# Kernel tuning notes

Measured on AMD Instinct MI355X. Metric: run time of the kernel, lower is better.

The kernel has to match this reference:

```python
import jax, jax.numpy as jnp
import numpy as np
from jax import lax

B, CIN, COUT, K, SDIM = 4, 64, 128, 3, 512
D = H = W = 48


def setup_inputs() -> dict:
    key = jax.random.key(0)
    ks = jax.random.split(key, 8)
    inv = lambda n: 1.0 / np.sqrt(n)
    return {
        "x": jax.random.normal(ks[0], (B, CIN, D, H, W), jnp.float32),
        "style": jax.random.normal(ks[1], (B, SDIM), jnp.float32),
        "weight": jax.random.normal(ks[2], (COUT, CIN, K, K, K), jnp.float32),
        "bias": jnp.zeros((COUT,), jnp.float32),
        "w_scale": jax.random.uniform(ks[3], (CIN, SDIM), jnp.float32, -inv(SDIM), inv(SDIM)),
        "b_scale": jnp.zeros((CIN,), jnp.float32),
        "w_shift": jax.random.uniform(ks[4], (CIN, SDIM), jnp.float32, -inv(SDIM), inv(SDIM)),
        "b_shift": jnp.zeros((CIN,), jnp.float32),
        "w_kmod": jax.random.uniform(ks[5], (CIN * K ** 3, SDIM), jnp.float32, -inv(SDIM), inv(SDIM)),
        "b_kmod": jnp.zeros((CIN * K ** 3,), jnp.float32),
    }


def reference(x, style, weight, bias, w_scale, b_scale, w_shift, b_shift, w_kmod, b_kmod):
    # style-based per-channel input modulation: x * (1+scale) + shift
    scale = style @ w_scale.T + b_scale          # [B, CIN]
    shift = style @ w_shift.T + b_shift          # [B, CIN]
    xm = x * (1.0 + scale)[:, :, None, None, None] + shift[:, :, None, None, None]
    # per-sample kernel modulation: weight * (1 + kmod)
    kmod = (style @ w_kmod.T + b_kmod).reshape(B, CIN, K, K, K)
    w = weight[None] * (1.0 + kmod[:, None])     # [B, COUT, CIN, K, K, K]

    def conv_one(xi, wi):
        # xi: [CIN, D, H, W], wi: [COUT, CIN, K, K, K]
        return lax.conv_general_dilated(
            xi[None], wi, window_strides=(1, 1, 1), padding="SAME",
            dimension_numbers=("NCDHW", "OIDHW", "NCDHW"))[0]

    out = jax.vmap(conv_one)(xm, w)              # [B, COUT, D, H, W]
    return out + bias[None, :, None, None, None]
```

## Files before the change

kernel.cpp:

```cpp
#include <hip/hip_runtime.h>
#include <hip/hip_bf16.h>

#define NB   4
#define CIN  64
#define COUT 128
#define SDIM 512
#define DIM  48
#define SP   (DIM*DIM*DIM)
#define TAPS 27
#define KTOT (CIN*TAPS)

#define WS_S1P 0
#define WS_SH  (WS_S1P + NB*CIN)
#define WS_KM  (WS_SH + NB*CIN)
#define XPB_OFF   32768ull
#define XPB_BYTES (4ull*125000ull*64ull*2ull)
#define WSBF_OFF  (XPB_OFF + XPB_BYTES)
#define WSBF_BYTES ((size_t)NB*27*8*128*8*2)

typedef __attribute__((ext_vector_type(4))) float  f32x4;
typedef __attribute__((ext_vector_type(8))) short  short8;
typedef __attribute__((ext_vector_type(8))) unsigned short u16x8;

__device__ __forceinline__ void gld16(const void* g, void* l) {
    __builtin_amdgcn_global_load_lds(
        (const __attribute__((address_space(1))) void*)g,
        (__attribute__((address_space(3))) void*)l, 16, 0, 0);
}

__global__ void modparams_kernel(const float* __restrict__ style,
                                 const float* __restrict__ w_scale, const float* __restrict__ b_scale,
                                 const float* __restrict__ w_shift, const float* __restrict__ b_shift,
                                 const float* __restrict__ w_kmod,  const float* __restrict__ b_kmod,
                                 float* __restrict__ ws) {
    const int ROWS = 2 * CIN + CIN * TAPS;
    int gwave = (blockIdx.x * blockDim.x + threadIdx.x) >> 6;
    int lane  = threadIdx.x & 63;
    if (gwave >= NB * ROWS) return;
    int b = gwave / ROWS;
    int r = gwave % ROWS;

    const float* srow = style + b * SDIM;
    const float* mrow;
    float bias, add = 0.f;
    float* dst;
    if (r < CIN) {
        mrow = w_scale + r * SDIM; bias = b_scale[r];
        dst = ws + WS_S1P + b * CIN + r; add = 1.f;
    } else if (r < 2 * CIN) {
        int c = r - CIN;
        mrow = w_shift + c * SDIM; bias = b_shift[c];
        dst = ws + WS_SH + b * CIN + c;
    } else {
        int t = r - 2 * CIN;
        mrow = w_kmod + t * SDIM; bias = b_kmod[t];
        dst = ws + WS_KM + b * (CIN * TAPS) + t;
    }

    const float4* s4 = (const float4*)srow;
    const float4* m4 = (const float4*)mrow;
    float acc = 0.f;
    #pragma unroll
    for (int k4 = 0; k4 < 2; ++k4) {
        float4 sv = s4[lane + k4 * 64];
        float4 mv = m4[lane + k4 * 64];
        acc += sv.x * mv.x + sv.y * mv.y + sv.z * mv.z + sv.w * mv.w;
    }
    #pragma unroll
    for (int off = 32; off; off >>= 1) acc += __shfl_down(acc, off);
    if (lane == 0) *dst = acc + bias + add;
}

__global__ void build_wsbf2_kernel(const float* __restrict__ weight, const float* __restrict__ ws,
                                   unsigned short* __restrict__ wsbf) {
    int d = blockIdx.x * blockDim.x + threadIdx.x;
    if (d >= NB * 27 * 8 * 128 * 8) return;
    int j   = d & 7;
    int o   = (d >> 3) & 127;
    int s   = (d >> 10) & 7;
    int rem = d >> 13;
    int tau = rem % 27;
    int b   = rem / 27;
    int c   = s * 8 + j;
    float wm = weight[(o * CIN + c) * TAPS + tau] * (1.f + ws[WS_KM + b * KTOT + c * TAPS + tau]);
    __hip_bfloat16 h = __float2bfloat16(wm);
    wsbf[d] = *(unsigned short*)&h;
}

__global__ __launch_bounds__(256) void pad_kernel(const float* __restrict__ x,
                                                  const float* __restrict__ ws,
                                                  unsigned short* __restrict__ xpb) {
    __shared__ unsigned short lxm[48 * 72];
    int bid = blockIdx.x;
    int py = bid % 50;
    int pz = (bid / 50) % 50;
    int b  = bid / 2500;
    int t = threadIdx.x;
    bool interior = (pz >= 1 && pz <= 48 && py >= 1 && py <= 48);
    if (interior) {
        int z = pz - 1, y = py - 1;
        const float* xr = x + (size_t)b * CIN * SP + (size_t)z * (DIM*DIM) + y * DIM;
        #pragma unroll
        for (int it = 0; it < 3; ++it) {
            int u = it * 256 + t;
            int c  = u / 12;
            int w4 = (u - c * 12) * 4;
            float4 v = *(const float4*)(xr + (size_t)c * SP + w4);
            float s1 = ws[WS_S1P + b * CIN + c];
            float sh = ws[WS_SH  + b * CIN + c];
            float m0 = v.x * s1 + sh, m1 = v.y * s1 + sh;
            float m2 = v.z * s1 + sh, m3 = v.w * s1 + sh;
            __hip_bfloat16 h0 = __float2bfloat16(m0);
            __hip_bfloat16 h1 = __float2bfloat16(m1);
            __hip_bfloat16 h2 = __float2bfloat16(m2);
            __hip_bfloat16 h3 = __float2bfloat16(m3);
            lxm[(w4 + 0) * 72 + c] = *(unsigned short*)&h0;
            lxm[(w4 + 1) * 72 + c] = *(unsigned short*)&h1;
            lxm[(w4 + 2) * 72 + c] = *(unsigned short*)&h2;
            lxm[(w4 + 3) * 72 + c] = *(unsigned short*)&h3;
        }
    }
    __syncthreads();
    unsigned short* dst = xpb + (size_t)b * 8000000ull + ((size_t)pz * 2500 + py * 50) * 64;
    #pragma unroll
    for (int it = 0; it < 2; ++it) {
        int i8 = it * 256 + t;
        if (i8 < 400) {
            int w  = i8 >> 3;
            int c8 = (i8 & 7) * 8;
            u16x8 v = {};
            if (interior && w >= 1 && w <= 48)
                v = *(const u16x8*)&lxm[(w - 1) * 72 + c8];
            *(u16x8*)(dst + i8 * 8) = v;
        }
    }
}

#define HALOPOS 600
#define BH_CHUNKS (HALOPOS*8)

#define GLD16R(dst, p, OFF)                                                    \
    asm volatile("global_load_dwordx4 %0, %1, off offset:" #OFF                \
                 : "=v"(dst) : "v"(p) : "memory")

#define ISSUEA(buf, tap_) do {                                                 \
    const unsigned short* _p0 = wA + (size_t)(tap_) * 8192;                    \
    const unsigned short* _p1 = _p0 + 4096;                                    \
    GLD16R(buf[0], _p0, 0);   GLD16R(buf[1], _p0, 256);                        \
    GLD16R(buf[2], _p0, 512); GLD16R(buf[3], _p0, 768);                        \
    GLD16R(buf[4], _p1, 0);   GLD16R(buf[5], _p1, 256);                        \
    GLD16R(buf[6], _p1, 512); GLD16R(buf[7], _p1, 768);                        \
} while (0)

#define DLT(t_) (((t_) / 9) * 100 + (((t_) / 3) % 3) * 10 + ((t_) % 3))

#define BREADX(dst, bb, t_) do {                                               \
    _Pragma("unroll")                                                          \
    for (int nf = 0; nf < 4; ++nf) {                                           \
        const int D = DLT(t_) + nf * 20;                                       \
        dst[nf] = *(const short8*)((const char*)Bh + bb[D & 7] + D * 128);     \
    }                                                                          \
} while (0)

#define TAPP(cur, nxt, bcur, bnxt, t_) do {                                    \
    if ((t_) < 26) {                                                           \
        ISSUEA(nxt, (t_) + 1);                                                 \
        asm volatile("s_waitcnt vmcnt(8)" ::: "memory");                       \
    } else {                                                                   \
        asm volatile("s_waitcnt vmcnt(0)" ::: "memory");                       \
    }                                                                          \
    __builtin_amdgcn_sched_barrier(0);                                         \
    BREADX(bC1, bb1, t_);                       \
    _Pragma("unroll")                                                          \
    for (int mf = 0; mf < 4; ++mf)                                             \
        _Pragma("unroll")                                                      \
        for (int nf = 0; nf < 4; ++nf)                                         \
            acc[mf][nf] = __builtin_amdgcn_mfma_f32_16x16x32_bf16(             \
                cur[mf], bcur[nf], acc[mf][nf], 0, 0, 0);                      \
    if ((t_) < 26) BREADX(bnxt, bb0, (t_) + 1);       \
    _Pragma("unroll")                                                          \
    for (int mf = 0; mf < 4; ++mf)                                             \
        _Pragma("unroll")                                                      \
        for (int nf = 0; nf < 4; ++nf)                                         \
            acc[mf][nf] = __builtin_amdgcn_mfma_f32_16x16x32_bf16(             \
                cur[4 + mf], bC1[nf], acc[mf][nf], 0, 0, 0);                   \
} while (0)

__global__ __launch_bounds__(512, 2) void conv_fast15_kernel(
    const unsigned short* __restrict__ xpb,
    const unsigned short* __restrict__ wsbf,
    const float* __restrict__ bias,
    float* __restrict__ out)
{
    __shared__ unsigned short Bh[HALOPOS * 64];

    const int t    = threadIdx.x;
    const int lane = t & 63;
    const int wid  = t >> 6;
    const int wz   = wid & 3;
    const int mh   = wid >> 2;

    int bid0 = blockIdx.x;
    int bid  = (bid0 & 7) * 216 + (bid0 >> 3);
    int tile = bid % 432;
    int b    = bid / 432;
    int tx = tile % 6;
    int ty = (tile / 6) % 6;
    int tz = tile / 36;
    int x0 = tx * 8, y0 = ty * 8, z0 = tz * 4;

    const unsigned short* xb = xpb + (size_t)b * 8000000ull;
    const unsigned short* wb = wsbf + (size_t)b * (27 * 8 * 128 * 8);

    const int col  = lane & 15;
    const int krow = lane >> 4;
    const int cy   = col >> 3;
    const int cx   = col & 7;
    const int pbase = wz * 100 + cy * 10 + cx;

    const unsigned short* wA = wb + (size_t)(krow * 128 + mh * 64 + col) * 8;

    unsigned bb0[8], bb1[8];
    #pragma unroll
    for (int j = 0; j < 8; ++j) {
        int pj = (pbase + j) & 7;
        bb0[j] = (unsigned)(pbase * 128 + ((krow ^ pj) << 4));
        bb1[j] = (unsigned)(pbase * 128 + (((4 + krow) ^ pj) << 4));
    }

    f32x4 acc[4][4] = {};
    short8 a0[8], a1[8];
    short8 bX[4], bY[4], bC1[4];

    ISSUEA(a0, 0);

    #pragma unroll
    for (int it = 0; it < 10; ++it) {
        int i = it * 512 + t;
        if (i < BH_CHUNKS) {
            int pidx = i >> 3;
            int slot = i & 7;
            int hx = pidx % 10;
            int hy = (pidx / 10) % 10;
            int hz = pidx / 100;
            int srcslot = slot ^ (pidx & 7);
            const unsigned short* g = xb
                + ((size_t)((z0 + hz) * 2500 + (y0 + hy) * 50 + (x0 + hx))) * 64
                + srcslot * 8;
            gld16(g, &Bh[i * 8]);
        }
    }
    __syncthreads();

    BREADX(bX, bb0, 0);

    #pragma unroll
    for (int tp = 0; tp < 26; tp += 2) {
        TAPP(a0, a1, bX, bY, tp);
        TAPP(a1, a0, bY, bX, tp + 1);
    }
    TAPP(a0, a1, bX, bY, 26);

    int z  = z0 + wz;
    int xx = x0 + cx;
    #pragma unroll
    for (int mf = 0; mf < 4; ++mf) {
        f32x4 bv = *(const f32x4*)&bias[mh * 64 + mf * 16 + krow * 4];
        #pragma unroll
        for (int nf = 0; nf < 4; ++nf) {
            int y = y0 + nf * 2 + cy;
            size_t p = (size_t)z * (DIM * DIM) + (size_t)y * DIM + xx;
            f32x4 a = acc[mf][nf];
            #pragma unroll
            for (int r = 0; r < 4; ++r) {
                int o = mh * 64 + mf * 16 + krow * 4 + r;
                out[(size_t)(b * COUT + o) * SP + p] = a[r] + bv[r];
            }
        }
    }
}

extern "C" void kernel_launch(void* const* d_in, const int* in_sizes, int n_in,
                              void* d_out, int out_size, void* d_ws, size_t ws_size,
                              hipStream_t stream) {
    const float* x       = (const float*)d_in[0];
    const float* style   = (const float*)d_in[1];
    const float* weight  = (const float*)d_in[2];
    const float* bias    = (const float*)d_in[3];
    const float* w_scale = (const float*)d_in[4];
    const float* b_scale = (const float*)d_in[5];
    const float* w_shift = (const float*)d_in[6];
    const float* b_shift = (const float*)d_in[7];
    const float* w_kmod  = (const float*)d_in[8];
    const float* b_kmod  = (const float*)d_in[9];
    float* out = (float*)d_out;
    float* ws  = (float*)d_ws;

    unsigned short* xpb  = (unsigned short*)((char*)d_ws + XPB_OFF);
    unsigned short* wsbf = (unsigned short*)((char*)d_ws + WSBF_OFF);

    {
        int waves = NB * (2 * CIN + CIN * TAPS);
        int blocks = (waves + 3) / 4;
        modparams_kernel<<<blocks, 256, 0, stream>>>(style, w_scale, b_scale,
                                                     w_shift, b_shift, w_kmod, b_kmod, ws);
    }
    {
        int n = NB * 27 * 8 * 128 * 8;
        build_wsbf2_kernel<<<(n + 255) / 256, 256, 0, stream>>>(weight, ws, wsbf);
    }
    {
        int blocks = NB * 50 * 50;
        pad_kernel<<<blocks, 256, 0, stream>>>(x, ws, xpb);
    }
    {
        int blocks = NB * 432;
        conv_fast15_kernel<<<blocks, 512, 0, stream>>>(xpb, wsbf, bias, out);
    }
}
```

Measured before the change: 217.6 us.

## Stage only half the input channels in LDS, load the rest from global

The conv kernel now stages only the first 32 input channels of the halo tile in shared memory. The second half of the B operand is fetched straight from global memory per tap and software-pipelined alongside the weight loads. This halves LDS footprint and staging traffic, which may allow more blocks per CU and a shorter prologue. The cost is extra global/L2 traffic and more outstanding vector memory ops and registers per tap.

New measurement: 348.6 us. 60.2% more time.

```diff
diff --git a/kernel.cpp b/kernel.cpp
--- a/kernel.cpp
+++ b/kernel.cpp
@@ -137,7 +137,7 @@
 }
 
 #define HALOPOS 600
-#define BH_CHUNKS (HALOPOS*8)
+#define BH_CHUNKS (HALOPOS*4)
 
 #define GLD16R(dst, p, OFF)                                                    \
     asm volatile("global_load_dwordx4 %0, %1, off offset:" #OFF                \
@@ -153,46 +153,55 @@
 } while (0)
 
 #define DLT(t_) (((t_) / 9) * 100 + (((t_) / 3) % 3) * 10 + ((t_) % 3))
-
-#define BREADX(dst, bb, t_) do {                                               \
+#define DLTGB(t_) ((((t_) / 9) * 2500 + (((t_) / 3) % 3) * 50 + ((t_) % 3)) * 128)
+
+#define ISSUEB1G(buf, tap_) do {                                               \
+    _Pragma("unroll")                                                          \
+    for (int nf = 0; nf < 4; ++nf) {                                           \
+        const char* _pg = (const char*)xw1p[nf] + DLTGB(tap_);                 \
+        GLD16R(buf[nf], _pg, 0);                                               \
+    }                                                                          \
+} while (0)
+
+#define BREADX(dst, t_) do {                                                   \
     _Pragma("unroll")                                                          \
     for (int nf = 0; nf < 4; ++nf) {                                           \
         const int D = DLT(t_) + nf * 20;                                       \
-        dst[nf] = *(const short8*)((const char*)Bh + bb[D & 7] + D * 128);     \
+        dst[nf] = *(const short8*)((const char*)Bh + bb0[D & 3] + D * 64);     \
     }                                                                          \
 } while (0)
 
-#define TAPP(cur, nxt, bcur, bnxt, t_) do {                                    \
+#define TAPP(curA, nxtA, bcur, bnxt, bGc, bGn, t_) do {                        \
     if ((t_) < 26) {                                                           \
-        ISSUEA(nxt, (t_) + 1);                                                 \
-        asm volatile("s_waitcnt vmcnt(8)" ::: "memory");                       \
+        ISSUEA(nxtA, (t_) + 1);                                                \
+        ISSUEB1G(bGn, (t_) + 1);                                               \
+        asm volatile("s_waitcnt vmcnt(12)" ::: "memory");                      \
     } else {                                                                   \
         asm volatile("s_waitcnt vmcnt(0)" ::: "memory");                       \
     }                                                                          \
     __builtin_amdgcn_sched_barrier(0);                                         \
-    BREADX(bC1, bb1, t_);                       \
     _Pragma("unroll")                                                          \
     for (int mf = 0; mf < 4; ++mf)                                             \
         _Pragma("unroll")                                                      \
         for (int nf = 0; nf < 4; ++nf)                                         \
             acc[mf][nf] = __builtin_amdgcn_mfma_f32_16x16x32_bf16(             \
-                cur[mf], bcur[nf], acc[mf][nf], 0, 0, 0);                      \
-    if ((t_) < 26) BREADX(bnxt, bb0, (t_) + 1);       \
+                curA[mf], bcur[nf], acc[mf][nf], 0, 0, 0);                     \
+    if ((t_) < 26) BREADX(bnxt, (t_) + 1);            \
     _Pragma("unroll")                                                          \
     for (int mf = 0; mf < 4; ++mf)                                             \
         _Pragma("unroll")                                                      \
         for (int nf = 0; nf < 4; ++nf)                                         \
             acc[mf][nf] = __builtin_amdgcn_mfma_f32_16x16x32_bf16(             \
-                cur[4 + mf], bC1[nf], acc[mf][nf], 0, 0, 0);                   \
+                curA[4 + mf], bGc[nf], acc[mf][nf], 0, 0, 0);                  \
 } while (0)
 
-__global__ __launch_bounds__(512, 2) void conv_fast15_kernel(
+__global__ __launch_bounds__(512, 2) void conv_fast18_kernel(
     const unsigned short* __restrict__ xpb,
     const unsigned short* __restrict__ wsbf,
     const float* __restrict__ bias,
     float* __restrict__ out)
 {
-    __shared__ unsigned short Bh[HALOPOS * 64];
+    __shared__ unsigned short Bh[HALOPOS * 32];
 
     const int t    = threadIdx.x;
     const int lane = t & 63;
@@ -220,30 +229,39 @@
 
     const unsigned short* wA = wb + (size_t)(krow * 128 + mh * 64 + col) * 8;
 
-    unsigned bb0[8], bb1[8];
-    #pragma unroll
-    for (int j = 0; j < 8; ++j) {
-        int pj = (pbase + j) & 7;
-        bb0[j] = (unsigned)(pbase * 128 + ((krow ^ pj) << 4));
-        bb1[j] = (unsigned)(pbase * 128 + (((4 + krow) ^ pj) << 4));
+    const unsigned short* xw1p[4];
+    #pragma unroll
+    for (int nf = 0; nf < 4; ++nf)
+        xw1p[nf] = xb
+            + ((size_t)(z0 + wz) * 2500
+               + (size_t)(y0 + cy + nf * 2) * 50
+               + (x0 + cx)) * 64
+            + (4 + krow) * 8;
+
+    unsigned bb0[4];
+    #pragma unroll
+    for (int j = 0; j < 4; ++j) {
+        int pj = (pbase + j) & 3;
+        bb0[j] = (unsigned)(pbase * 64 + ((krow ^ pj) << 4));
     }
 
     f32x4 acc[4][4] = {};
     short8 a0[8], a1[8];
-    short8 bX[4], bY[4], bC1[4];
+    short8 bX[4], bY[4], bGa[4], bGb[4];
 
     ISSUEA(a0, 0);
-
-    #pragma unroll
-    for (int it = 0; it < 10; ++it) {
+    ISSUEB1G(bGa, 0);
+
+    #pragma unroll
+    for (int it = 0; it < 5; ++it) {
         int i = it * 512 + t;
         if (i < BH_CHUNKS) {
-            int pidx = i >> 3;
-            int slot = i & 7;
+            int pidx = i >> 2;
+            int slot = i & 3;
             int hx = pidx % 10;
             int hy = (pidx / 10) % 10;
             int hz = pidx / 100;
-            int srcslot = slot ^ (pidx & 7);
+            int srcslot = slot ^ (pidx & 3);
             const unsigned short* g = xb
                 + ((size_t)((z0 + hz) * 2500 + (y0 + hy) * 50 + (x0 + hx))) * 64
                 + srcslot * 8;
@@ -252,14 +270,14 @@
     }
     __syncthreads();
 
-    BREADX(bX, bb0, 0);
+    BREADX(bX, 0);
 
     #pragma unroll
     for (int tp = 0; tp < 26; tp += 2) {
-        TAPP(a0, a1, bX, bY, tp);
-        TAPP(a1, a0, bY, bX, tp + 1);
-    }
-    TAPP(a0, a1, bX, bY, 26);
+        TAPP(a0, a1, bX, bY, bGa, bGb, tp);
+        TAPP(a1, a0, bY, bX, bGb, bGa, tp + 1);
+    }
+    TAPP(a0, a1, bX, bY, bGa, bGb, 26);
 
     int z  = z0 + wz;
     int xx = x0 + cx;
@@ -315,6 +333,6 @@
     }
     {
         int blocks = NB * 432;
-        conv_fast15_kernel<<<blocks, 512, 0, stream>>>(xpb, wsbf, bias, out);
-    }
-}
+        conv_fast18_kernel<<<blocks, 512, 0, stream>>>(xpb, wsbf, bias, out);
+    }
+}
```
